# Performance work log

Measured on AMD Instinct MI355X. Metric: run time of the kernel, lower is better.

## Reference

```python
import jax, jax.numpy as jnp
import numpy as np

EPS_SN = 1e-12
EPS_BN = 1e-5
NEG_SLOPE = 0.01  # nn.LeakyReLU default


def _l2n(v):
    return v / (jnp.linalg.norm(v) + EPS_SN)


def _sn_weight(w, u, v):
    # one power iteration (as in SpectralNorm._update_u_v), u/v are buffers
    h = w.shape[0]
    W2 = w.reshape(h, -1)
    Wd = jax.lax.stop_gradient(W2)
    v = _l2n(Wd.T @ u)
    u = _l2n(Wd @ v)
    sigma = u @ (W2 @ v)  # gradient flows through W2 only
    return w / sigma


def _conv(x, w, pad):
    return jax.lax.conv_general_dilated(
        x, w, window_strides=(1, 1), padding=[(pad, pad), (pad, pad)],
        dimension_numbers=('NCHW', 'OIHW', 'NCHW'))


def _bn(x, scale, bias):
    # BatchNorm2d in training mode: biased batch stats over (B,H,W)
    mean = x.mean(axis=(0, 2, 3), keepdims=True)
    var = x.var(axis=(0, 2, 3), keepdims=True)
    xn = (x - mean) * jax.lax.rsqrt(var + EPS_BN)
    return xn * scale[None, :, None, None] + bias[None, :, None, None]


def setup_inputs() -> dict:
    key = jax.random.key(0)
    ks = jax.random.split(key, 16)
    B, C, W, H = 2, 256, 64, 64
    Cq = C // 4
    inp = {
        'x': jax.random.normal(ks[0], (B, C, W, H), jnp.float32),
        'pre': jax.random.normal(ks[1], (B, C, W, H), jnp.float32),
        'mask': (jax.random.uniform(ks[2], (B, 1, W, H)) > 0.5).astype(jnp.float32),
        'q_w': jax.random.normal(ks[3], (Cq, C, 1, 1), jnp.float32) * 0.02,
        'gamma': jnp.array(0.5, jnp.float32),
        'alpha': jnp.array(0.5, jnp.float32),
        'bn1_s': jnp.ones((2 * C,), jnp.float32),
        'bn1_b': jnp.zeros((2 * C,), jnp.float32),
        'c1_w': jax.random.normal(ks[4], (C, 2 * C, 3, 3), jnp.float32) * 0.02,
        'u1': _l2n(jax.random.normal(ks[5], (C,), jnp.float32)),
        'v1': _l2n(jax.random.normal(ks[6], (2 * C * 9,), jnp.float32)),
        'bn2_s': jnp.ones((C,), jnp.float32),
        'bn2_b': jnp.zeros((C,), jnp.float32),
        'c2_w': jax.random.normal(ks[7], (C, C, 3, 3), jnp.float32) * 0.02,
        'u2': _l2n(jax.random.normal(ks[8], (C,), jnp.float32)),
        'v2': _l2n(jax.random.normal(ks[9], (C * 9,), jnp.float32)),
        'by_w': jax.random.normal(ks[10], (C, 2 * C, 1, 1), jnp.float32) * 0.02,
        'u3': _l2n(jax.random.normal(ks[11], (C,), jnp.float32)),
        'v3': _l2n(jax.random.normal(ks[12], (2 * C,), jnp.float32)),
    }
    return inp


def reference(x, pre, mask, q_w, gamma, alpha, bn1_s, bn1_b, c1_w, u1, v1,
              bn2_s, bn2_b, c2_w, u2, v2, by_w, u3, v3):
    B, C, W, H = x.shape
    N = W * H
    q = _conv(x, q_w, 0).reshape(B, -1, N)
    energy = jnp.einsum('bcn,bcm->bnm', q, q)       # B x N x N (query == key)
    attention = jax.nn.softmax(energy, axis=-1)
    val = x.reshape(B, C, N)
    # torch.bmm(value, attention^T): out[b,c,j] = sum_k val[b,c,k] * attn[b,j,k]
    out = jnp.einsum('bck,bjk->bcj', val, attention).reshape(B, C, W, H)
    out = gamma * out + x

    context_flow = jnp.einsum('bck,bjk->bcj', pre.reshape(B, -1, N), attention)
    context_flow = context_flow.reshape(B, -1, W, H)
    context_flow = alpha * (1 - mask) * context_flow + mask * pre

    y = jnp.concatenate([out, context_flow], axis=1)  # B x 2C x W x H
    # ResBlock(2C -> C, hidden C, BatchNorm, spectral norm, sample_type='none')
    h = jax.nn.leaky_relu(_bn(y, bn1_s, bn1_b), NEG_SLOPE)
    h = _conv(h, _sn_weight(c1_w, u1, v1), 1)
    h = jax.nn.leaky_relu(_bn(h, bn2_s, bn2_b), NEG_SLOPE)
    h = _conv(h, _sn_weight(c2_w, u2, v2), 1)
    sc = _conv(y, _sn_weight(by_w, u3, v3), 0)
    res = h + sc
    return res, attention
```

## Files before the change

kernel.cpp:

```cpp
#include <hip/hip_runtime.h>
#include <cstddef>


typedef __attribute__((ext_vector_type(8))) short bh8;
typedef __attribute__((ext_vector_type(4))) short bh4;
typedef __attribute__((ext_vector_type(4))) float f4;

static __device__ __forceinline__ short f2bf(float f) {
  unsigned u = __float_as_uint(f);
  unsigned r = (u + 0x7fffu + ((u >> 16) & 1u)) >> 16;
  return (short)r;
}
static __device__ __forceinline__ float bf2f(unsigned short s) {
  return __uint_as_float(((unsigned)s) << 16);
}

__device__ __forceinline__ float blk_sum256(float v, float* sm) {
#pragma unroll
  for (int o = 32; o > 0; o >>= 1) v += __shfl_down(v, o, 64);
  __syncthreads();
  if ((threadIdx.x & 63) == 0) sm[threadIdx.x >> 6] = v;
  __syncthreads();
  return sm[0] + sm[1] + sm[2] + sm[3];
}

__device__ __forceinline__ float blk_max256(float v, float* sm) {
#pragma unroll
  for (int o = 32; o > 0; o >>= 1) v = fmaxf(v, __shfl_down(v, o, 64));
  __syncthreads();
  if ((threadIdx.x & 63) == 0) sm[threadIdx.x >> 6] = v;
  __syncthreads();
  return fmaxf(fmaxf(sm[0], sm[1]), fmaxf(sm[2], sm[3]));
}

#define SWCOL(row, col) ((col) ^ ((((row) >> 1) & 3) << 3))

__global__ __launch_bounds__(256) void snA_kernel(
    const float* __restrict__ w1, const float* __restrict__ u1,
    const float* __restrict__ w2, const float* __restrict__ u2,
    const float* __restrict__ w3, const float* __restrict__ u3,
    float* __restrict__ t1, float* __restrict__ t2, float* __restrict__ t3) {
  int g = blockIdx.x * 256 + threadIdx.x;
  const float* W; const float* u; float* t; int K; int j;
  if (g < 4608)      { W = w1; u = u1; t = t1; K = 4608; j = g; }
  else if (g < 6912) { W = w2; u = u2; t = t2; K = 2304; j = g - 4608; }
  else if (g < 7424) { W = w3; u = u3; t = t3; K = 512;  j = g - 6912; }
  else return;
  float a = 0.f;
  for (int i = 0; i < 256; ++i) a += W[(size_t)i * K + j] * u[i];
  t[j] = a;
}

__global__ __launch_bounds__(256) void snN_kernel(
    const float* __restrict__ t1, const float* __restrict__ t2,
    const float* __restrict__ t3, float* __restrict__ invn) {
  __shared__ float red[4];
  const float* t; int K;
  if (blockIdx.x == 0)      { t = t1; K = 4608; }
  else if (blockIdx.x == 1) { t = t2; K = 2304; }
  else                      { t = t3; K = 512;  }
  float ss = 0.f;
  for (int j = threadIdx.x; j < K; j += 256) { float v = t[j]; ss += v * v; }
  ss = blk_sum256(ss, red);
  if (threadIdx.x == 0) invn[blockIdx.x] = 1.0f / (sqrtf(ss) + 1e-12f);
}

__global__ __launch_bounds__(256) void snB_kernel(
    const float* __restrict__ w1, const float* __restrict__ t1,
    const float* __restrict__ w2, const float* __restrict__ t2,
    const float* __restrict__ w3, const float* __restrict__ t3,
    float* __restrict__ st) {
  int blk = blockIdx.x;
  int w = blk >> 6;
  const float* W; const float* t; int K;
  if (w == 0)      { W = w1; t = t1; K = 4608; }
  else if (w == 1) { W = w2; t = t2; K = 2304; }
  else             { W = w3; t = t3; K = 512;  }
  int lane = threadIdx.x & 63, wave = threadIdx.x >> 6;
  int row = (blk & 63) * 4 + wave;
  const float* Wr = W + (size_t)row * K;
  float a = 0.f;
  for (int j = lane; j < K; j += 64) a += Wr[j] * t[j];
#pragma unroll
  for (int o = 32; o > 0; o >>= 1) a += __shfl_down(a, o, 64);
  if (lane == 0) st[w * 256 + row] = a;
}

__global__ __launch_bounds__(256) void snC_kernel(
    const float* __restrict__ st, const float* __restrict__ invn,
    float* __restrict__ inv_sig) {
  __shared__ float red[4];
  int w = blockIdx.x;
  float v = st[w * 256 + threadIdx.x];
  float ss = blk_sum256(v * v, red);
  if (threadIdx.x == 0) {
    float in = invn[w];
    float s2 = in * in * ss;
    float sn = in * sqrtf(ss);
    float sigma = s2 / (sn + 1e-12f);
    inv_sig[w] = 1.0f / sigma;
  }
}

__global__ __launch_bounds__(256) void cast_xp_kernel(
    const float* __restrict__ x, const float* __restrict__ pre,
    unsigned short* __restrict__ xb, unsigned short* __restrict__ pb) {
  int i = blockIdx.x * 256 + threadIdx.x;
  const float* s = blockIdx.y ? pre : x;
  unsigned short* d = blockIdx.y ? pb : xb;
  float4 v0 = ((const float4*)s)[i * 2];
  float4 v1 = ((const float4*)s)[i * 2 + 1];
  bh8 o = { f2bf(v0.x), f2bf(v0.y), f2bf(v0.z), f2bf(v0.w),
            f2bf(v1.x), f2bf(v1.y), f2bf(v1.z), f2bf(v1.w) };
  *(bh8*)&d[(size_t)i * 8] = o;
}

__global__ __launch_bounds__(256) void transpose_w_kernel(
    const float* __restrict__ src, unsigned short* __restrict__ dst, int Cin) {
  int i = blockIdx.x * 256 + threadIdx.x;
  int ci = i % Cin;
  int co = (i / Cin) & 255;
  int t = i / (Cin * 256);
  dst[i] = (unsigned short)f2bf(src[((size_t)co * Cin + ci) * 9 + t]);
}

__global__ __launch_bounds__(256) void cast_w3_kernel(
    const float* __restrict__ src, unsigned short* __restrict__ dst) {
  int i = blockIdx.x * 256 + threadIdx.x;
  float4 v0 = ((const float4*)src)[i * 2];
  float4 v1 = ((const float4*)src)[i * 2 + 1];
  bh8 o = { f2bf(v0.x), f2bf(v0.y), f2bf(v0.z), f2bf(v0.w),
            f2bf(v1.x), f2bf(v1.y), f2bf(v1.z), f2bf(v1.w) };
  *(bh8*)&dst[(size_t)i * 8] = o;
}

__global__ __launch_bounds__(256) void qconv_kernel(
    const float* __restrict__ x, const float* __restrict__ qw, float* __restrict__ q) {
  int gid = blockIdx.x;
  int ntile = gid & 15;
  int cq = (gid >> 4) & 63;
  int b = gid >> 10;
  int n = (ntile << 8) + threadIdx.x;
  const float* xb = x + ((size_t)b << 20) + n;
  const float* wr = qw + cq * 256;
  float acc = 0.f;
#pragma unroll 8
  for (int c = 0; c < 256; ++c) acc += wr[c] * xb[(size_t)c << 12];
  q[(((size_t)(b * 64 + cq)) << 12) + n] = acc;
}

__global__ __launch_bounds__(256) void qtrans_kernel(
    const float* __restrict__ q, unsigned short* __restrict__ qt) {
  int b = blockIdx.y;
  int n0 = blockIdx.x * 64;
  __shared__ float t[64][65];
  int tid = threadIdx.x;
  int col = tid & 63, krow = tid >> 6;
#pragma unroll
  for (int p = 0; p < 16; ++p) {
    int k = p * 4 + krow;
    t[k][col] = q[(((size_t)(b * 64 + k)) << 12) + n0 + col];
  }
  __syncthreads();
#pragma unroll
  for (int p = 0; p < 16; ++p) {
    int r = p * 4 + krow;
    qt[(((size_t)(b * 4096 + n0 + r)) << 6) + col] = (unsigned short)f2bf(t[col][r]);
  }
}

__global__ __launch_bounds__(256, 4) void energy_mfma_kernel(
    const unsigned short* __restrict__ qt, float* __restrict__ att) {
  int b = blockIdx.z;
  int n0 = blockIdx.x << 7;
  int m0 = blockIdx.y << 7;
  __shared__ short Qn[128 * 64];
  __shared__ short Qm[128 * 64];
  int tid = threadIdx.x;
  int wave = tid >> 6, lane = tid & 63;
  int ln = lane & 15, qd = lane >> 4;
  int wy = wave >> 1, wx = wave & 1;
  int g = tid & 7, row0 = tid >> 3;
#pragma unroll
  for (int it = 0; it < 4; ++it) {
    int r = row0 + it * 32;
    int colb = ((g ^ (r & 7)) << 3);
    *(bh8*)&Qn[(r << 6) + colb] =
        *(const bh8*)&qt[((size_t)(b * 4096 + n0 + r) << 6) + (g << 3)];
    *(bh8*)&Qm[(r << 6) + colb] =
        *(const bh8*)&qt[((size_t)(b * 4096 + m0 + r) << 6) + (g << 3)];
  }
  __syncthreads();
  f4 z = {0.f, 0.f, 0.f, 0.f};
  f4 acc[4][4];
#pragma unroll
  for (int i = 0; i < 4; ++i)
#pragma unroll
    for (int j = 0; j < 4; ++j) acc[i][j] = z;
#pragma unroll
  for (int kc = 0; kc < 2; ++kc) {
    bh8 am[4];
#pragma unroll
    for (int j = 0; j < 4; ++j) {
      int row = wx * 64 + j * 16 + ln;
      int colb = (((qd + (kc << 2)) ^ (row & 7)) << 3);
      am[j] = *(const bh8*)&Qm[(row << 6) + colb];
    }
#pragma unroll
    for (int i = 0; i < 4; ++i) {
      int row = wy * 64 + i * 16 + ln;
      int colb = (((qd + (kc << 2)) ^ (row & 7)) << 3);
      bh8 an = *(const bh8*)&Qn[(row << 6) + colb];
#pragma unroll
      for (int j = 0; j < 4; ++j)
        acc[i][j] = __builtin_amdgcn_mfma_f32_16x16x32_bf16(an, am[j], acc[i][j], 0, 0, 0);
    }
  }
  size_t base = ((size_t)b << 24);
#pragma unroll
  for (int i = 0; i < 4; ++i) {
    int n = n0 + wy * 64 + i * 16 + qd * 4;
#pragma unroll
    for (int j = 0; j < 4; ++j) {
      int m = m0 + wx * 64 + j * 16 + ln;
#pragma unroll
      for (int r = 0; r < 4; ++r)
        att[base + (((size_t)(n + r)) << 12) + m] = acc[i][j][r];
    }
  }
}

__global__ __launch_bounds__(256) void softmax_kernel(float* __restrict__ att) {
  __shared__ float red[4];
  size_t row = blockIdx.x;
  float4* rp4 = (float4*)(att + (row << 12));
  int tid = threadIdx.x;
  float4 v[4];
#pragma unroll
  for (int i = 0; i < 4; ++i) v[i] = rp4[tid + (i << 8)];
  float mx = -INFINITY;
#pragma unroll
  for (int i = 0; i < 4; ++i)
    mx = fmaxf(mx, fmaxf(fmaxf(v[i].x, v[i].y), fmaxf(v[i].z, v[i].w)));
  mx = blk_max256(mx, red);
  float s = 0.f;
#pragma unroll
  for (int i = 0; i < 4; ++i) {
    v[i].x = __expf(v[i].x - mx); v[i].y = __expf(v[i].y - mx);
    v[i].z = __expf(v[i].z - mx); v[i].w = __expf(v[i].w - mx);
    s += v[i].x + v[i].y + v[i].z + v[i].w;
  }
  s = blk_sum256(s, red);
  float inv = 1.0f / s;
#pragma unroll
  for (int i = 0; i < 4; ++i) {
    v[i].x *= inv; v[i].y *= inv; v[i].z *= inv; v[i].w *= inv;
    rp4[tid + (i << 8)] = v[i];
  }
}

__global__ __launch_bounds__(256, 2) void outcf_mfma_kernel(
    const unsigned short* __restrict__ xb, const unsigned short* __restrict__ pb,
    const float* __restrict__ x, const float* __restrict__ pre,
    const float* __restrict__ att, const float* __restrict__ mask,
    const float* __restrict__ gamma_p, const float* __restrict__ alpha_p,
    unsigned short* __restrict__ y_t) {
  int b = blockIdx.z;
  int c0 = blockIdx.y * 64;
  int j0 = blockIdx.x * 64;
  __shared__ short smem[12 * 64 * 32];
  int tid = threadIdx.x;
  int wave = tid >> 6, lane = tid & 63;
  short* Xs = smem + wave * (3 * 2048);
  short* Ps = Xs + 2048;
  short* As = Ps + 2048;
  int ln = lane & 15, qd = lane >> 4;
  f4 z = {0.f, 0.f, 0.f, 0.f};
  f4 accO[4][4], accC[4][4];
#pragma unroll
  for (int i = 0; i < 4; ++i)
#pragma unroll
    for (int j = 0; j < 4; ++j) { accO[i][j] = z; accC[i][j] = z; }
  int part = lane & 3, r4 = lane >> 2;
  int part8 = lane & 7, r8 = lane >> 3;
  int kb = wave << 10;
  for (int it = 0; it < 32; ++it) {
    int k0 = kb + (it << 5);
#pragma unroll
    for (int t2 = 0; t2 < 4; ++t2) {
      int rr = r4 + t2 * 16;
      int col = SWCOL(rr, part * 8);
      bh8 xv = *(const bh8*)&xb[((size_t)(b * 256 + c0 + rr) << 12) + k0 + part * 8];
      bh8 pv = *(const bh8*)&pb[((size_t)(b * 256 + c0 + rr) << 12) + k0 + part * 8];
      *(bh8*)&Xs[rr * 32 + col] = xv;
      *(bh8*)&Ps[rr * 32 + col] = pv;
    }
#pragma unroll
    for (int t2 = 0; t2 < 8; ++t2) {
      int rr = r8 + t2 * 8;
      int col = SWCOL(rr, part8 * 4);
      float4 v = *(const float4*)&att[((size_t)b << 24) + ((size_t)(j0 + rr) << 12) + k0 + part8 * 4];
      bh4 o = { f2bf(v.x), f2bf(v.y), f2bf(v.z), f2bf(v.w) };
      *(bh4*)&As[rr * 32 + col] = o;
    }
    bh8 bf[4];
#pragma unroll
    for (int j = 0; j < 4; ++j) {
      int row = j * 16 + ln;
      bf[j] = *(const bh8*)&As[row * 32 + SWCOL(row, qd * 8)];
    }
#pragma unroll
    for (int i = 0; i < 4; ++i) {
      int row = i * 16 + ln;
      int col = SWCOL(row, qd * 8);
      bh8 ax = *(const bh8*)&Xs[row * 32 + col];
      bh8 ap = *(const bh8*)&Ps[row * 32 + col];
#pragma unroll
      for (int j = 0; j < 4; ++j) {
        accO[i][j] = __builtin_amdgcn_mfma_f32_16x16x32_bf16(ax, bf[j], accO[i][j], 0, 0, 0);
        accC[i][j] = __builtin_amdgcn_mfma_f32_16x16x32_bf16(ap, bf[j], accC[i][j], 0, 0, 0);
      }
    }
  }
  float* red = (float*)smem;
  __syncthreads();
#pragma unroll
  for (int j = 0; j < 4; ++j) {
    if (j == wave) continue;
    int s = wave - (wave > j ? 1 : 0);
#pragma unroll
    for (int i = 0; i < 4; ++i)
      *(f4*)&red[((((j * 3 + s) << 2) + i) << 8) + (lane << 2)] = accO[i][j];
  }
  __syncthreads();
#pragma unroll
  for (int j = 0; j < 4; ++j) {
    if (j != wave) continue;
#pragma unroll
    for (int s = 0; s < 3; ++s)
#pragma unroll
      for (int i = 0; i < 4; ++i) {
        f4 v = *(const f4*)&red[((((j * 3 + s) << 2) + i) << 8) + (lane << 2)];
        accO[i][j][0] += v[0]; accO[i][j][1] += v[1];
        accO[i][j][2] += v[2]; accO[i][j][3] += v[3];
      }
  }
  __syncthreads();
#pragma unroll
  for (int j = 0; j < 4; ++j) {
    if (j == wave) continue;
    int s = wave - (wave > j ? 1 : 0);
#pragma unroll
    for (int i = 0; i < 4; ++i)
      *(f4*)&red[((((j * 3 + s) << 2) + i) << 8) + (lane << 2)] = accC[i][j];
  }
  __syncthreads();
#pragma unroll
  for (int j = 0; j < 4; ++j) {
    if (j != wave) continue;
#pragma unroll
    for (int s = 0; s < 3; ++s)
#pragma unroll
      for (int i = 0; i < 4; ++i) {
        f4 v = *(const f4*)&red[((((j * 3 + s) << 2) + i) << 8) + (lane << 2)];
        accC[i][j][0] += v[0]; accC[i][j][1] += v[1];
        accC[i][j][2] += v[2]; accC[i][j][3] += v[3];
      }
  }
  float g = gamma_p[0], al = alpha_p[0];
#pragma unroll
  for (int j = 0; j < 4; ++j) {
    if (j != wave) continue;
    int jp = j0 + j * 16 + ln;
    float mv = mask[(b << 12) + jp];
#pragma unroll
    for (int i = 0; i < 4; ++i) {
      int cb = c0 + i * 16 + qd * 4;
      bh4 oY, oC;
#pragma unroll
      for (int r = 0; r < 4; ++r) {
        float xo = x[((size_t)(b * 256 + cb + r) << 12) + jp];
        float po = pre[((size_t)(b * 256 + cb + r) << 12) + jp];
        oY[r] = f2bf(g * accO[i][j][r] + xo);
        oC[r] = f2bf(al * (1.f - mv) * accC[i][j][r] + mv * po);
      }
      size_t rowb = ((size_t)b * 4096 + jp) * 512;
      *(bh4*)&y_t[rowb + cb] = oY;
      *(bh4*)&y_t[rowb + 256 + cb] = oC;
    }
  }
}

__global__ __launch_bounds__(256) void bn_part_kernel(
    const void* __restrict__ src, int isbf, int C, int rows_per_slab,
    float* __restrict__ part) {
  int slab = blockIdx.x;
  int r0 = slab * rows_per_slab;
  for (int co = threadIdx.x; co < C; co += 256) {
    float s = 0.f, ss = 0.f;
    if (isbf) {
      const unsigned short* p = (const unsigned short*)src;
      for (int r = 0; r < rows_per_slab; ++r) {
        float v = bf2f(p[(size_t)(r0 + r) * C + co]); s += v; ss += v * v;
      }
    } else {
      const float* p = (const float*)src;
      for (int r = 0; r < rows_per_slab; ++r) {
        float v = p[(size_t)(r0 + r) * C + co]; s += v; ss += v * v;
      }
    }
    part[(size_t)(slab * 2) * C + co] = s;
    part[(size_t)(slab * 2 + 1) * C + co] = ss;
  }
}

__global__ __launch_bounds__(256) void bn_finish_kernel(
    const float* __restrict__ part, int C, int slabs, float inv_count,
    float* __restrict__ mean, float* __restrict__ rstd) {
  for (int co = threadIdx.x; co < C; co += 256) {
    float s = 0.f, ss = 0.f;
    for (int sl = 0; sl < slabs; ++sl) {
      s += part[(size_t)(sl * 2) * C + co];
      ss += part[(size_t)(sl * 2 + 1) * C + co];
    }
    float m = s * inv_count;
    float var = ss * inv_count - m * m;
    mean[co] = m;
    rstd[co] = rsqrtf(var + 1e-5f);
  }
}

__global__ __launch_bounds__(256) void bn_act_bf_kernel(
    const unsigned short* __restrict__ src, unsigned short* __restrict__ dst,
    const float* __restrict__ mean, const float* __restrict__ rstd,
    const float* __restrict__ sc, const float* __restrict__ bi, int Cm1) {
  int i = blockIdx.x * 256 + threadIdx.x;
  int ch = (i * 4) & Cm1;
  bh4 v = *(const bh4*)&src[(size_t)i * 4];
  bh4 o;
#pragma unroll
  for (int e = 0; e < 4; ++e) {
    int c = ch + e;
    float a = rstd[c] * sc[c];
    float bb = bi[c] - mean[c] * a;
    float f = bf2f((unsigned short)v[e]) * a + bb;
    f = f > 0.f ? f : 0.01f * f;
    o[e] = f2bf(f);
  }
  *(bh4*)&dst[(size_t)i * 4] = o;
}

__global__ __launch_bounds__(256) void bn_act_f_kernel(
    const float* __restrict__ src, unsigned short* __restrict__ dst,
    const float* __restrict__ mean, const float* __restrict__ rstd,
    const float* __restrict__ sc, const float* __restrict__ bi, int Cm1) {
  int i = blockIdx.x * 256 + threadIdx.x;
  int ch = (i * 4) & Cm1;
  float4 v = ((const float4*)src)[i];
  float vv[4] = {v.x, v.y, v.z, v.w};
  bh4 o;
#pragma unroll
  for (int e = 0; e < 4; ++e) {
    int c = ch + e;
    float a = rstd[c] * sc[c];
    float bb = bi[c] - mean[c] * a;
    float f = vv[e] * a + bb;
    f = f > 0.f ? f : 0.01f * f;
    o[e] = f2bf(f);
  }
  *(bh4*)&dst[(size_t)i * 4] = o;
}

__global__ __launch_bounds__(256, 3) void conv3x3_mfma_kernel(
    const unsigned short* __restrict__ act_t, const unsigned short* __restrict__ wt,
    const float* __restrict__ inv_sig, int sidx, int Cin, int mode,
    float* __restrict__ out) {
  int b = blockIdx.z;
  int co0 = blockIdx.y * 64;
  int n0 = blockIdx.x * 64;
  __shared__ short smem[4 * 194 * 32];
  int tid = threadIdx.x;
  int wave = tid >> 6, lane = tid & 63;
  short* act_s = smem + wave * (194 * 32);
  int ln = lane & 15, qd = lane >> 4;
  int part = lane & 3, r4 = lane >> 2;
  f4 z = {0.f, 0.f, 0.f, 0.f};
  f4 acc[4][4];
#pragma unroll
  for (int i = 0; i < 4; ++i)
#pragma unroll
    for (int j = 0; j < 4; ++j) acc[i][j] = z;
  bh8 zf = {};
  int nchunk = Cin >> 5;
  int per = nchunk >> 2;
  for (int itc = 0; itc < per; ++itc) {
    int cc = wave * per + itc;
    int ci0 = cc << 5;
#pragma unroll
    for (int it = 0; it < 13; ++it) {
      int rr = r4 + it * 16;
      if (rr < 194) {
        int flat = n0 - 65 + rr;
        bh8 v = {};
        if ((unsigned)flat < 4096u)
          v = *(const bh8*)&act_t[((size_t)(b * 4096 + flat)) * Cin + ci0 + part * 8];
        *(bh8*)&act_s[rr * 32 + SWCOL(rr, part * 8)] = v;
      }
    }
#pragma unroll
    for (int t = 0; t < 9; ++t) {
      int dy = t / 3, dx = t - dy * 3;
      int off = (dy - 1) * 64 + (dx - 1);
      bh8 bw[4];
#pragma unroll
      for (int j = 0; j < 4; ++j) {
        int co = co0 + j * 16 + ln;
        bw[j] = *(const bh8*)&wt[((size_t)(t * 256 + co)) * Cin + ci0 + qd * 8];
      }
#pragma unroll
      for (int i = 0; i < 4; ++i) {
        int px = i * 16 + ln;
        int row = 65 + off + px;
        bh8 a = *(const bh8*)&act_s[row * 32 + SWCOL(row, qd * 8)];
        if (dx == 0 && px == 0) a = zf;
        if (dx == 2 && px == 63) a = zf;
#pragma unroll
        for (int j = 0; j < 4; ++j)
          acc[i][j] = __builtin_amdgcn_mfma_f32_16x16x32_bf16(a, bw[j], acc[i][j], 0, 0, 0);
      }
    }
  }
  float* red = (float*)smem;
  __syncthreads();
#pragma unroll
  for (int j = 0; j < 4; ++j) {
    if (j == wave) continue;
    int s = wave - (wave > j ? 1 : 0);
#pragma unroll
    for (int i = 0; i < 4; ++i)
      *(f4*)&red[((((j * 3 + s) << 2) + i) << 8) + (lane << 2)] = acc[i][j];
  }
  __syncthreads();
#pragma unroll
  for (int j = 0; j < 4; ++j) {
    if (j != wave) continue;
#pragma unroll
    for (int s = 0; s < 3; ++s)
#pragma unroll
      for (int i = 0; i < 4; ++i) {
        f4 v = *(const f4*)&red[((((j * 3 + s) << 2) + i) << 8) + (lane << 2)];
        acc[i][j][0] += v[0]; acc[i][j][1] += v[1];
        acc[i][j][2] += v[2]; acc[i][j][3] += v[3];
      }
  }
  float isg = inv_sig[sidx];
  if (mode == 0) {
#pragma unroll
    for (int j = 0; j < 4; ++j) {
      if (j != wave) continue;
      int co = co0 + j * 16 + ln;
#pragma unroll
      for (int i = 0; i < 4; ++i) {
        int pb = n0 + i * 16 + qd * 4;
#pragma unroll
        for (int r = 0; r < 4; ++r)
          out[((size_t)(b * 4096 + pb + r)) * 256 + co] = acc[i][j][r] * isg;
      }
    }
  } else {
#pragma unroll
    for (int j = 0; j < 4; ++j) {
      if (j != wave) continue;
      int co = co0 + j * 16 + ln;
#pragma unroll
      for (int i = 0; i < 4; ++i) {
        int pb = n0 + i * 16 + qd * 4;
        float4* rp = (float4*)&out[((size_t)(b * 256 + co) << 12) + pb];
        float4 v = *rp;
        v.x += acc[i][j][0] * isg; v.y += acc[i][j][1] * isg;
        v.z += acc[i][j][2] * isg; v.w += acc[i][j][3] * isg;
        *rp = v;
      }
    }
  }
}

__global__ __launch_bounds__(256, 3) void scgemm_mfma_kernel(
    const unsigned short* __restrict__ y_t, const unsigned short* __restrict__ w3b,
    const float* __restrict__ inv_sig, float* __restrict__ res) {
  int b = blockIdx.z;
  int co0 = blockIdx.y * 64;
  int n0 = blockIdx.x * 64;
  __shared__ short smem[24576];
  int tid = threadIdx.x;
  int wave = tid >> 6, lane = tid & 63;
  short* Ys = smem + wave * 2048;
  int ln = lane & 15, qd = lane >> 4;
  int part = lane & 3, r4 = lane >> 2;
  f4 z = {0.f, 0.f, 0.f, 0.f};
  f4 acc[4][4];
#pragma unroll
  for (int i = 0; i < 4; ++i)
#pragma unroll
    for (int j = 0; j < 4; ++j) acc[i][j] = z;
  int kb = wave << 7;
#pragma unroll
  for (int it = 0; it < 4; ++it) {
    int k0 = kb + (it << 5);
#pragma unroll
    for (int t2 = 0; t2 < 4; ++t2) {
      int rr = r4 + t2 * 16;
      bh8 v = *(const bh8*)&y_t[((size_t)(b * 4096 + n0 + rr)) * 512 + k0 + part * 8];
      *(bh8*)&Ys[rr * 32 + SWCOL(rr, part * 8)] = v;
    }
    bh8 bw[4];
#pragma unroll
    for (int j = 0; j < 4; ++j)
      bw[j] = *(const bh8*)&w3b[((size_t)(co0 + j * 16 + ln)) * 512 + k0 + qd * 8];
#pragma unroll
    for (int i = 0; i < 4; ++i) {
      int row = i * 16 + ln;
      bh8 a = *(const bh8*)&Ys[row * 32 + SWCOL(row, qd * 8)];
#pragma unroll
      for (int j = 0; j < 4; ++j)
        acc[i][j] = __builtin_amdgcn_mfma_f32_16x16x32_bf16(a, bw[j], acc[i][j], 0, 0, 0);
    }
  }
  float* red = (float*)smem;
  __syncthreads();
#pragma unroll
  for (int j = 0; j < 4; ++j) {
    if (j == wave) continue;
    int s = wave - (wave > j ? 1 : 0);
#pragma unroll
    for (int i = 0; i < 4; ++i)
      *(f4*)&red[((((j * 3 + s) << 2) + i) << 8) + (lane << 2)] = acc[i][j];
  }
  __syncthreads();
#pragma unroll
  for (int j = 0; j < 4; ++j) {
    if (j != wave) continue;
#pragma unroll
    for (int s = 0; s < 3; ++s)
#pragma unroll
      for (int i = 0; i < 4; ++i) {
        f4 v = *(const f4*)&red[((((j * 3 + s) << 2) + i) << 8) + (lane << 2)];
        acc[i][j][0] += v[0]; acc[i][j][1] += v[1];
        acc[i][j][2] += v[2]; acc[i][j][3] += v[3];
      }
  }
  float isg = inv_sig[2];
#pragma unroll
  for (int j = 0; j < 4; ++j) {
    if (j != wave) continue;
    int co = co0 + j * 16 + ln;
#pragma unroll
    for (int i = 0; i < 4; ++i) {
      int pb = n0 + i * 16 + qd * 4;
      float4 o;
      o.x = acc[i][j][0] * isg; o.y = acc[i][j][1] * isg;
      o.z = acc[i][j][2] * isg; o.w = acc[i][j][3] * isg;
      *(float4*)&res[((size_t)(b * 256 + co) << 12) + pb] = o;
    }
  }
}

extern "C" void kernel_launch(void* const* d_in, const int* in_sizes, int n_in,
                              void* d_out, int out_size, void* d_ws, size_t ws_size,
                              hipStream_t stream) {
  const float* x     = (const float*)d_in[0];
  const float* pre   = (const float*)d_in[1];
  const float* mask  = (const float*)d_in[2];
  const float* qw    = (const float*)d_in[3];
  const float* gamma = (const float*)d_in[4];
  const float* alpha = (const float*)d_in[5];
  const float* bn1s  = (const float*)d_in[6];
  const float* bn1b  = (const float*)d_in[7];
  const float* c1w   = (const float*)d_in[8];
  const float* u1    = (const float*)d_in[9];
  const float* bn2s  = (const float*)d_in[11];
  const float* bn2b  = (const float*)d_in[12];
  const float* c2w   = (const float*)d_in[13];
  const float* u2    = (const float*)d_in[14];
  const float* byw   = (const float*)d_in[16];
  const float* u3    = (const float*)d_in[17];

  float* res = (float*)d_out;
  float* att = res + (size_t)2 * 256 * 4096;

  char* W = (char*)d_ws;
  float* inv_sig = (float*)(W + 0);
  float* mean1   = (float*)(W + 64);
  float* rstd1   = (float*)(W + 2112);
  float* mean2   = (float*)(W + 4160);
  float* rstd2   = (float*)(W + 5184);
  float* part    = (float*)(W + 8192);
  float* q       = (float*)(W + 270336);
  unsigned short* x_bf = (unsigned short*)(W + 2367488);
  unsigned short* p_bf = (unsigned short*)(W + 6561792);
  unsigned short* y_t  = (unsigned short*)(W + 10756096);
  unsigned short* act1 = (unsigned short*)(W + 19144704);
  float* h1_t          = (float*)(W + 27533312);
  unsigned short* act2 = (unsigned short*)(W + 35921920);
  unsigned short* w1t  = (unsigned short*)(W + 40116224);
  unsigned short* w2t  = (unsigned short*)(W + 42475520);
  unsigned short* w3b  = (unsigned short*)(W + 43655168);
  float* t1      = (float*)(W + 43917312);
  float* t2      = (float*)(W + 43935744);
  float* t3      = (float*)(W + 43944960);
  float* invn    = (float*)(W + 43947008);
  float* st      = (float*)(W + 43947072);
  unsigned short* qt = (unsigned short*)(W + 19144704);

  hipLaunchKernelGGL(snA_kernel, dim3(29), dim3(256), 0, stream,
                     c1w, u1, c2w, u2, byw, u3, t1, t2, t3);
  hipLaunchKernelGGL(snN_kernel, dim3(3), dim3(256), 0, stream, t1, t2, t3, invn);
  hipLaunchKernelGGL(snB_kernel, dim3(192), dim3(256), 0, stream,
                     c1w, t1, c2w, t2, byw, t3, st);
  hipLaunchKernelGGL(snC_kernel, dim3(3), dim3(256), 0, stream, st, invn, inv_sig);
  hipLaunchKernelGGL(cast_xp_kernel, dim3(1024, 2), dim3(256), 0, stream, x, pre, x_bf, p_bf);
  hipLaunchKernelGGL(transpose_w_kernel, dim3(4608), dim3(256), 0, stream, c1w, w1t, 512);
  hipLaunchKernelGGL(transpose_w_kernel, dim3(2304), dim3(256), 0, stream, c2w, w2t, 256);
  hipLaunchKernelGGL(cast_w3_kernel, dim3(64), dim3(256), 0, stream, byw, w3b);
  hipLaunchKernelGGL(qconv_kernel, dim3(2048), dim3(256), 0, stream, x, qw, q);
  hipLaunchKernelGGL(qtrans_kernel, dim3(64, 2), dim3(256), 0, stream, q, qt);
  hipLaunchKernelGGL(energy_mfma_kernel, dim3(32, 32, 2), dim3(256), 0, stream, qt, att);
  hipLaunchKernelGGL(softmax_kernel, dim3(8192), dim3(256), 0, stream, att);
  hipLaunchKernelGGL(outcf_mfma_kernel, dim3(64, 4, 2), dim3(256), 0, stream,
                     x_bf, p_bf, x, pre, att, mask, gamma, alpha, y_t);
  hipLaunchKernelGGL(bn_part_kernel, dim3(64), dim3(256), 0, stream,
                     (const void*)y_t, 1, 512, 128, part);
  hipLaunchKernelGGL(bn_finish_kernel, dim3(1), dim3(256), 0, stream,
                     part, 512, 64, 1.0f / 8192.0f, mean1, rstd1);
  hipLaunchKernelGGL(bn_act_bf_kernel, dim3(8192), dim3(256), 0, stream,
                     y_t, act1, mean1, rstd1, bn1s, bn1b, 511);
  hipLaunchKernelGGL(conv3x3_mfma_kernel, dim3(64, 4, 2), dim3(256), 0, stream,
                     act1, w1t, inv_sig, 0, 512, 0, h1_t);
  hipLaunchKernelGGL(bn_part_kernel, dim3(64), dim3(256), 0, stream,
                     (const void*)h1_t, 0, 256, 128, part);
  hipLaunchKernelGGL(bn_finish_kernel, dim3(1), dim3(256), 0, stream,
                     part, 256, 64, 1.0f / 8192.0f, mean2, rstd2);
  hipLaunchKernelGGL(bn_act_f_kernel, dim3(2048), dim3(256), 0, stream,
                     h1_t, act2, mean2, rstd2, bn2s, bn2b, 255);
  hipLaunchKernelGGL(scgemm_mfma_kernel, dim3(64, 4, 2), dim3(256), 0, stream,
                     y_t, w3b, inv_sig, res);
  hipLaunchKernelGGL(conv3x3_mfma_kernel, dim3(64, 4, 2), dim3(256), 0, stream,
                     act2, w2t, inv_sig, 1, 256, 1, res);
}
```

Before: 691.4 us.

## Register-prefetch next K-chunk in attention-apply, conv3x3 and shortcut GEMM kernels

Adds software pipelining: global loads for the next K chunk (activations, attention rows, weights) are issued into registers before the MFMA work on the current chunk, hiding global memory latency. The 3x3 conv weight layout is changed to chunk-major [t][cc][co][32] so each chunk's weight slice is contiguous. Launch bounds drop from 3 to 2 blocks per SM to leave room for the extra prefetch registers, at the cost of lower occupancy.

```diff
diff --git a/kernel.cpp b/kernel.cpp
--- a/kernel.cpp
+++ b/kernel.cpp
@@ -118,9 +118,13 @@
 __global__ __launch_bounds__(256) void transpose_w_kernel(
     const float* __restrict__ src, unsigned short* __restrict__ dst, int Cin) {
   int i = blockIdx.x * 256 + threadIdx.x;
-  int ci = i % Cin;
-  int co = (i / Cin) & 255;
-  int t = i / (Cin * 256);
+  int ciin = i & 31;
+  int co = (i >> 5) & 255;
+  int rest = i >> 13;
+  int nchunk = Cin >> 5;
+  int cc = rest % nchunk;
+  int t = rest / nchunk;
+  int ci = (cc << 5) + ciin;
   dst[i] = (unsigned short)f2bf(src[((size_t)co * Cin + ci) * 9 + t]);
 }
 
@@ -284,24 +288,49 @@
   int part = lane & 3, r4 = lane >> 2;
   int part8 = lane & 7, r8 = lane >> 3;
   int kb = wave << 10;
+  bh8 xr[4], pr[4];
+  float4 ar[8];
+#pragma unroll
+  for (int t2 = 0; t2 < 4; ++t2) {
+    int rr = r4 + t2 * 16;
+    xr[t2] = *(const bh8*)&xb[((size_t)(b * 256 + c0 + rr) << 12) + kb + part * 8];
+    pr[t2] = *(const bh8*)&pb[((size_t)(b * 256 + c0 + rr) << 12) + kb + part * 8];
+  }
+#pragma unroll
+  for (int t2 = 0; t2 < 8; ++t2) {
+    int rr = r8 + t2 * 8;
+    ar[t2] = *(const float4*)&att[((size_t)b << 24) + ((size_t)(j0 + rr) << 12) + kb + part8 * 4];
+  }
   for (int it = 0; it < 32; ++it) {
     int k0 = kb + (it << 5);
 #pragma unroll
     for (int t2 = 0; t2 < 4; ++t2) {
       int rr = r4 + t2 * 16;
       int col = SWCOL(rr, part * 8);
-      bh8 xv = *(const bh8*)&xb[((size_t)(b * 256 + c0 + rr) << 12) + k0 + part * 8];
-      bh8 pv = *(const bh8*)&pb[((size_t)(b * 256 + c0 + rr) << 12) + k0 + part * 8];
-      *(bh8*)&Xs[rr * 32 + col] = xv;
-      *(bh8*)&Ps[rr * 32 + col] = pv;
+      *(bh8*)&Xs[rr * 32 + col] = xr[t2];
+      *(bh8*)&Ps[rr * 32 + col] = pr[t2];
     }
 #pragma unroll
     for (int t2 = 0; t2 < 8; ++t2) {
       int rr = r8 + t2 * 8;
       int col = SWCOL(rr, part8 * 4);
-      float4 v = *(const float4*)&att[((size_t)b << 24) + ((size_t)(j0 + rr) << 12) + k0 + part8 * 4];
+      float4 v = ar[t2];
       bh4 o = { f2bf(v.x), f2bf(v.y), f2bf(v.z), f2bf(v.w) };
       *(bh4*)&As[rr * 32 + col] = o;
+    }
+    if (it + 1 < 32) {
+      int k1 = k0 + 32;
+#pragma unroll
+      for (int t2 = 0; t2 < 4; ++t2) {
+        int rr = r4 + t2 * 16;
+        xr[t2] = *(const bh8*)&xb[((size_t)(b * 256 + c0 + rr) << 12) + k1 + part * 8];
+        pr[t2] = *(const bh8*)&pb[((size_t)(b * 256 + c0 + rr) << 12) + k1 + part * 8];
+      }
+#pragma unroll
+      for (int t2 = 0; t2 < 8; ++t2) {
+        int rr = r8 + t2 * 8;
+        ar[t2] = *(const float4*)&att[((size_t)b << 24) + ((size_t)(j0 + rr) << 12) + k1 + part8 * 4];
+      }
     }
     bh8 bf[4];
 #pragma unroll
@@ -471,7 +500,7 @@
   *(bh4*)&dst[(size_t)i * 4] = o;
 }
 
-__global__ __launch_bounds__(256, 3) void conv3x3_mfma_kernel(
+__global__ __launch_bounds__(256, 2) void conv3x3_mfma_kernel(
     const unsigned short* __restrict__ act_t, const unsigned short* __restrict__ wt,
     const float* __restrict__ inv_sig, int sidx, int Cin, int mode,
     float* __restrict__ out) {
@@ -493,30 +522,57 @@
   bh8 zf = {};
   int nchunk = Cin >> 5;
   int per = nchunk >> 2;
+  size_t tstride = (size_t)nchunk * 256 * 32;
+  int cc0 = wave * per;
+  bh8 sreg[13];
+#pragma unroll
+  for (int it = 0; it < 13; ++it) {
+    int rr = r4 + it * 16;
+    bh8 v = {};
+    if (rr < 194) {
+      int flat = n0 - 65 + rr;
+      if ((unsigned)flat < 4096u)
+        v = *(const bh8*)&act_t[((size_t)(b * 4096 + flat)) * Cin + (cc0 << 5) + part * 8];
+    }
+    sreg[it] = v;
+  }
   for (int itc = 0; itc < per; ++itc) {
-    int cc = wave * per + itc;
-    int ci0 = cc << 5;
+    int cc = cc0 + itc;
 #pragma unroll
     for (int it = 0; it < 13; ++it) {
       int rr = r4 + it * 16;
-      if (rr < 194) {
-        int flat = n0 - 65 + rr;
+      if (rr < 194)
+        *(bh8*)&act_s[rr * 32 + SWCOL(rr, part * 8)] = sreg[it];
+    }
+    if (itc + 1 < per) {
+      int ci0n = (cc + 1) << 5;
+#pragma unroll
+      for (int it = 0; it < 13; ++it) {
+        int rr = r4 + it * 16;
         bh8 v = {};
-        if ((unsigned)flat < 4096u)
-          v = *(const bh8*)&act_t[((size_t)(b * 4096 + flat)) * Cin + ci0 + part * 8];
-        *(bh8*)&act_s[rr * 32 + SWCOL(rr, part * 8)] = v;
-      }
-    }
+        if (rr < 194) {
+          int flat = n0 - 65 + rr;
+          if ((unsigned)flat < 4096u)
+            v = *(const bh8*)&act_t[((size_t)(b * 4096 + flat)) * Cin + ci0n + part * 8];
+        }
+        sreg[it] = v;
+      }
+    }
+    const unsigned short* wb0 = wt + ((size_t)cc * 256) * 32;
+    bh8 bwc[4], bwn[4];
+#pragma unroll
+    for (int j = 0; j < 4; ++j)
+      bwc[j] = *(const bh8*)&wb0[(size_t)(co0 + j * 16 + ln) * 32 + qd * 8];
 #pragma unroll
     for (int t = 0; t < 9; ++t) {
+      if (t < 8) {
+        const unsigned short* wbn = wb0 + (size_t)(t + 1) * tstride;
+#pragma unroll
+        for (int j = 0; j < 4; ++j)
+          bwn[j] = *(const bh8*)&wbn[(size_t)(co0 + j * 16 + ln) * 32 + qd * 8];
+      }
       int dy = t / 3, dx = t - dy * 3;
       int off = (dy - 1) * 64 + (dx - 1);
-      bh8 bw[4];
-#pragma unroll
-      for (int j = 0; j < 4; ++j) {
-        int co = co0 + j * 16 + ln;
-        bw[j] = *(const bh8*)&wt[((size_t)(t * 256 + co)) * Cin + ci0 + qd * 8];
-      }
 #pragma unroll
       for (int i = 0; i < 4; ++i) {
         int px = i * 16 + ln;
@@ -526,7 +582,11 @@
         if (dx == 2 && px == 63) a = zf;
 #pragma unroll
         for (int j = 0; j < 4; ++j)
-          acc[i][j] = __builtin_amdgcn_mfma_f32_16x16x32_bf16(a, bw[j], acc[i][j], 0, 0, 0);
+          acc[i][j] = __builtin_amdgcn_mfma_f32_16x16x32_bf16(a, bwc[j], acc[i][j], 0, 0, 0);
+      }
+      if (t < 8) {
+#pragma unroll
+        for (int j = 0; j < 4; ++j) bwc[j] = bwn[j];
       }
     }
   }
@@ -585,7 +645,7 @@
   }
 }
 
-__global__ __launch_bounds__(256, 3) void scgemm_mfma_kernel(
+__global__ __launch_bounds__(256, 2) void scgemm_mfma_kernel(
     const unsigned short* __restrict__ y_t, const unsigned short* __restrict__ w3b,
     const float* __restrict__ inv_sig, float* __restrict__ res) {
   int b = blockIdx.z;
@@ -604,26 +664,47 @@
 #pragma unroll
     for (int j = 0; j < 4; ++j) acc[i][j] = z;
   int kb = wave << 7;
+  bh8 ys[4], bwc[4], yn[4], bwn[4];
+#pragma unroll
+  for (int t2 = 0; t2 < 4; ++t2) {
+    int rr = r4 + t2 * 16;
+    ys[t2] = *(const bh8*)&y_t[((size_t)(b * 4096 + n0 + rr)) * 512 + kb + part * 8];
+  }
+#pragma unroll
+  for (int j = 0; j < 4; ++j)
+    bwc[j] = *(const bh8*)&w3b[((size_t)(co0 + j * 16 + ln)) * 512 + kb + qd * 8];
 #pragma unroll
   for (int it = 0; it < 4; ++it) {
     int k0 = kb + (it << 5);
 #pragma unroll
     for (int t2 = 0; t2 < 4; ++t2) {
       int rr = r4 + t2 * 16;
-      bh8 v = *(const bh8*)&y_t[((size_t)(b * 4096 + n0 + rr)) * 512 + k0 + part * 8];
-      *(bh8*)&Ys[rr * 32 + SWCOL(rr, part * 8)] = v;
-    }
-    bh8 bw[4];
-#pragma unroll
-    for (int j = 0; j < 4; ++j)
-      bw[j] = *(const bh8*)&w3b[((size_t)(co0 + j * 16 + ln)) * 512 + k0 + qd * 8];
+      *(bh8*)&Ys[rr * 32 + SWCOL(rr, part * 8)] = ys[t2];
+    }
+    if (it < 3) {
+      int k1 = k0 + 32;
+#pragma unroll
+      for (int t2 = 0; t2 < 4; ++t2) {
+        int rr = r4 + t2 * 16;
+        yn[t2] = *(const bh8*)&y_t[((size_t)(b * 4096 + n0 + rr)) * 512 + k1 + part * 8];
+      }
+#pragma unroll
+      for (int j = 0; j < 4; ++j)
+        bwn[j] = *(const bh8*)&w3b[((size_t)(co0 + j * 16 + ln)) * 512 + k1 + qd * 8];
+    }
 #pragma unroll
     for (int i = 0; i < 4; ++i) {
       int row = i * 16 + ln;
       bh8 a = *(const bh8*)&Ys[row * 32 + SWCOL(row, qd * 8)];
 #pragma unroll
       for (int j = 0; j < 4; ++j)
-        acc[i][j] = __builtin_amdgcn_mfma_f32_16x16x32_bf16(a, bw[j], acc[i][j], 0, 0, 0);
+        acc[i][j] = __builtin_amdgcn_mfma_f32_16x16x32_bf16(a, bwc[j], acc[i][j], 0, 0, 0);
+    }
+    if (it < 3) {
+#pragma unroll
+      for (int t2 = 0; t2 < 4; ++t2) ys[t2] = yn[t2];
+#pragma unroll
+      for (int j = 0; j < 4; ++j) bwc[j] = bwn[j];
     }
   }
   float* red = (float*)smem;
```

After: 607.6 us. -12.1%, faster.
